# Optimization experiments

Measured on AMD Instinct MI355X. Metric: run time of the kernel, lower is better.

## Reference

```python
import jax, jax.numpy as jnp
import numpy as np

B, T, D = 16, 2048, 512  # batch, max timesteps, input_size == output_size
H = D                    # output_size


def setup_inputs() -> dict:
    key = jax.random.key(0)
    k1, k2, k3, k4 = jax.random.split(key, 4)
    x = jax.random.normal(k1, (B, T, D), dtype=jnp.float32)
    lengths = jax.random.randint(k2, (B,), 1, T + 1)
    lengths = jnp.sort(lengths)[::-1].at[0].set(T)  # descending, max == T (pack_padded contract)
    W_in = jax.random.normal(k3, (6 * H, D), dtype=jnp.float32) * (1.0 / np.sqrt(D))
    b_in = jax.random.normal(k4, (6 * H,), dtype=jnp.float32) * 0.01
    return {"x": x, "lengths": lengths, "W_in": W_in, "b_in": b_in}


def reference(x, lengths, W_in, b_in):
    # Faithful to the given source: input_linearity is applied to BOTH the
    # timestep input and the previous hidden state (requires input_size == output_size).
    Bx, Tx, Dx = x.shape
    Wt = W_in.T  # [D, 6H]

    xt_all = jnp.transpose(x, (1, 0, 2))                               # [T, B, D]
    mask_all = (jnp.arange(Tx)[:, None] < lengths[None, :])            # [T, B]

    def step(carry, inputs):
        h, c = carry                 # [B, H] each
        x_t, mask = inputs           # [B, D], [B]
        pi = x_t @ Wt + b_in         # [B, 6H]
        ps = h @ Wt + b_in           # [B, 6H]  (input_linearity on state, per source)
        g = pi[:, :5 * H] + ps[:, :5 * H]
        i_g = jax.nn.sigmoid(g[:, 0 * H:1 * H])
        f_g = jax.nn.sigmoid(g[:, 1 * H:2 * H])
        m_i = jnp.tanh(g[:, 2 * H:3 * H])
        o_g = jax.nn.sigmoid(g[:, 3 * H:4 * H])
        hw_g = jax.nn.sigmoid(g[:, 4 * H:5 * H])
        mem = i_g * m_i + f_g * c
        out = o_g * jnp.tanh(mem)
        out = hw_g * out + (1.0 - hw_g) * pi[:, 5 * H:6 * H]
        m = mask[:, None].astype(x.dtype)
        out = out * m                # padded rows produce 0, state zeroed (matches source)
        mem = mem * m
        return (out, mem), out

    h0 = jnp.zeros((Bx, H), dtype=x.dtype)
    c0 = jnp.zeros((Bx, H), dtype=x.dtype)
    _, outs = jax.lax.scan(step, (h0, c0), (xt_all, mask_all))  # outs: [T, B, H]
    return jnp.transpose(outs, (1, 0, 2))                       # [B, T, H] padded output
```

## Files before the change

kernel.cpp:

```cpp
#include <hip/hip_runtime.h>


#define NG 64
#define BLK 256
#define BB 16
#define TT 2048
#define DD 512
#define HHH 512
#define CC 8

typedef _Float16 f16;
typedef _Float16 f16x4 __attribute__((ext_vector_type(4)));
typedef _Float16 f16x8 __attribute__((ext_vector_type(8)));
typedef float f32x4 __attribute__((ext_vector_type(4)));
typedef unsigned long long u64;

__device__ __forceinline__ float sigf(float v) {
  return 1.0f / (1.0f + __expf(-v));
}
__device__ __forceinline__ float tanhfast(float v) {
  return 2.0f / (1.0f + __expf(-2.0f * v)) - 1.0f;
}

__device__ __forceinline__ f16 h_lo(u64 w) {
  return __builtin_bit_cast(f16, (unsigned short)(w & 0xffffu));
}
__device__ __forceinline__ f16 h_hi(u64 w) {
  return __builtin_bit_cast(f16, (unsigned short)((w >> 16) & 0xffffu));
}

__global__ __launch_bounds__(BLK, 1) void lstm_scan(
    const float* __restrict__ x, const int* __restrict__ lengths,
    const float* __restrict__ W, const float* __restrict__ bias,
    float* __restrict__ out,
    u64* __restrict__ hex , int repmask) {
  __shared__ f16 u_sw[BB * DD];
  __shared__ f16 h_sw[BB * DD];
  __shared__ float gbuf[4 * 16 * 17];
  __shared__ float cbuf[BB * CC];

  const int tid = threadIdx.x;
  const int wg = blockIdx.x;
  const int wave = tid >> 6;
  const int lane = tid & 63;
  const int q = lane >> 4;
  const int n16 = lane & 15;
  const int nrep = repmask + 1;

  f16x8 bW[16];
  {
    int grow = 0;
    bool valid = true;
    if (wave < 3) {
      int gate = 2 * wave + (n16 >> 3);
      grow = gate * HHH + wg * CC + (n16 & 7);
    } else if (n16 < 8) {
      grow = 5 * HHH + wg * CC + n16;
    } else {
      valid = false;
    }
    const float* wr = W + (size_t)grow * DD;
#pragma unroll
    for (int kk = 0; kk < 16; ++kk) {
      f16x8 v;
      if (valid) {
        const float* p = wr + kk * 32 + q * 8;
#pragma unroll
        for (int j = 0; j < 8; ++j) v[j] = (f16)p[j];
      } else {
#pragma unroll
        for (int j = 0; j < 8; ++j) v[j] = (f16)0.0f;
      }
      bW[kk] = v;
    }
  }

  int soffv[8], pidx[8];
  size_t xcm[8];
#pragma unroll
  for (int i = 0; i < 8; ++i) {
    int e = (tid + i * BLK) * 4;
    int m = e >> 9;
    int k = e & 511;
    pidx[i] = m * 256 + (k >> 1);
    xcm[i] = (size_t)m * TT * DD + k;
    int kk = k >> 5, qq = (k >> 3) & 3, j0 = k & 7;
    int L = qq * 16 + m;
    soffv[i] = (kk * 64 + (L ^ kk)) * 8 + j0;
  }

  const int eb = tid >> 3;
  const int en = tid & 7;
  float bb0 = 0, bb1 = 0, bb2 = 0, bb3 = 0, bb4 = 0, bb5 = 0;
  int mylen = 0;
  if (tid < 128) {
    int gc = wg * CC + en;
    bb0 = bias[0 * HHH + gc];
    bb1 = bias[1 * HHH + gc];
    bb2 = bias[2 * HHH + gc];
    bb3 = bias[3 * HHH + gc];
    bb4 = bias[4 * HHH + gc];
    bb5 = bias[5 * HHH + gc];
    mylen = lengths[eb];
    cbuf[tid] = 0.0f;
  }

  u64* const myrep = hex + (size_t)(wg & repmask) * 8192;

  f32x4 xv[8];
#pragma unroll
  for (int i = 0; i < 8; ++i) xv[i] = *(const f32x4*)(x + xcm[i]);

  __syncthreads();

  for (int t = 0; t < TT; ++t) {
    const u64* hb = myrep + (size_t)(t & 1) * 4096;
    const unsigned wtag = (unsigned)t;
    u64 w0[8], w1[8];
    for (;;) {
#pragma unroll
      for (int i = 0; i < 8; ++i) {
        w0[i] = __hip_atomic_load(hb + pidx[i], __ATOMIC_RELAXED,
                                  __HIP_MEMORY_SCOPE_AGENT);
        w1[i] = __hip_atomic_load(hb + pidx[i] + 1, __ATOMIC_RELAXED,
                                  __HIP_MEMORY_SCOPE_AGENT);
      }
      unsigned bad = 0;
#pragma unroll
      for (int i = 0; i < 8; ++i)
        bad |= ((unsigned)(w0[i] >> 32) ^ wtag) |
               ((unsigned)(w1[i] >> 32) ^ wtag);
      if (bad == 0) break;
    }

#pragma unroll
    for (int i = 0; i < 8; ++i) {
      f16x4 hv;
      hv[0] = h_lo(w0[i]);
      hv[1] = h_hi(w0[i]);
      hv[2] = h_lo(w1[i]);
      hv[3] = h_hi(w1[i]);
      f16x4 uv;
#pragma unroll
      for (int j = 0; j < 4; ++j) uv[j] = (f16)xv[i][j] + hv[j];
      *(f16x4*)(u_sw + soffv[i]) = uv;
      *(f16x4*)(h_sw + soffv[i]) = hv;
    }
    __syncthreads();

    f32x4 acc0 = {0.f, 0.f, 0.f, 0.f}, acc1 = {0.f, 0.f, 0.f, 0.f};
    f32x4 acc2 = {0.f, 0.f, 0.f, 0.f}, acc3 = {0.f, 0.f, 0.f, 0.f};
    const f16* asrc = (wave < 3) ? u_sw : h_sw;
#pragma unroll
    for (int kk = 0; kk < 16; kk += 4) {
      f16x8 a0 = *(const f16x8*)(asrc + (kk * 64 + (lane ^ kk)) * 8);
      f16x8 a1 =
          *(const f16x8*)(asrc + ((kk + 1) * 64 + (lane ^ (kk + 1))) * 8);
      f16x8 a2 =
          *(const f16x8*)(asrc + ((kk + 2) * 64 + (lane ^ (kk + 2))) * 8);
      f16x8 a3 =
          *(const f16x8*)(asrc + ((kk + 3) * 64 + (lane ^ (kk + 3))) * 8);
      acc0 = __builtin_amdgcn_mfma_f32_16x16x32_f16(a0, bW[kk], acc0, 0, 0, 0);
      acc1 =
          __builtin_amdgcn_mfma_f32_16x16x32_f16(a1, bW[kk + 1], acc1, 0, 0, 0);
      acc2 =
          __builtin_amdgcn_mfma_f32_16x16x32_f16(a2, bW[kk + 2], acc2, 0, 0, 0);
      acc3 =
          __builtin_amdgcn_mfma_f32_16x16x32_f16(a3, bW[kk + 3], acc3, 0, 0, 0);
    }
#pragma unroll
    for (int r = 0; r < 4; ++r)
      gbuf[wave * 272 + (q * 4 + r) * 17 + n16] =
          (acc0[r] + acc1[r]) + (acc2[r] + acc3[r]);
    __syncthreads();

    if (tid < 128) {
      float g0 = gbuf[0 * 272 + eb * 17 + en] + 2.f * bb0;
      float g1 = gbuf[0 * 272 + eb * 17 + en + 8] + 2.f * bb1;
      float g2 = gbuf[1 * 272 + eb * 17 + en] + 2.f * bb2;
      float g3 = gbuf[1 * 272 + eb * 17 + en + 8] + 2.f * bb3;
      float g4 = gbuf[2 * 272 + eb * 17 + en] + 2.f * bb4;
      float p5 = gbuf[2 * 272 + eb * 17 + en + 8];
      float qv = gbuf[3 * 272 + eb * 17 + en];
      float ig = sigf(g0), fg = sigf(g1), mt = tanhfast(g2);
      float og = sigf(g3), hwv = sigf(g4);
      float pi5 = p5 - qv + bb5;
      float cold = cbuf[tid];
      float mem = ig * mt + fg * cold;
      float o1 = og * tanhfast(mem);
      float ov = hwv * o1 + (1.0f - hwv) * pi5;
      float msk = (t < mylen) ? 1.0f : 0.0f;
      ov *= msk;
      mem *= msk;
      cbuf[tid] = mem;

      unsigned hbits =
          (unsigned)__builtin_bit_cast(unsigned short, (f16)ov);
      unsigned other = (unsigned)__shfl_xor((int)hbits, 1, 64);
      u64 wv;
      if ((en & 1) == 0)
        wv = (u64)(hbits & 0xffffu) | ((u64)(other & 0xffffu) << 16) |
             ((u64)(unsigned)(t + 1) << 32);
      else
        wv = (u64)(other & 0xffffu) | ((u64)(hbits & 0xffffu) << 16) |
             ((u64)(unsigned)(t + 1) << 32);
      const int rh = (nrep + 1) >> 1;
      const int rs = (en & 1) ? rh : 0;
      const int re = (en & 1) ? nrep : rh;
      u64* pdst = hex + (size_t)rs * 8192 + (size_t)((t + 1) & 1) * 4096 +
                  eb * 256 + wg * 4 + (en >> 1);
      for (int r = rs; r < re; ++r) {
        __hip_atomic_store(pdst, wv, __ATOMIC_RELAXED,
                           __HIP_MEMORY_SCOPE_AGENT);
        pdst += 8192;
      }
      out[((size_t)eb * TT + t) * HHH + wg * CC + en] = ov;
    }

    if (t + 1 < TT) {
#pragma unroll
      for (int i = 0; i < 8; ++i)
        xv[i] = *(const f32x4*)(x + xcm[i] + (size_t)(t + 1) * DD);
    }
  }
}

extern "C" void kernel_launch(void* const* d_in, const int* in_sizes, int n_in,
                              void* d_out, int out_size, void* d_ws,
                              size_t ws_size, hipStream_t stream) {
  (void)in_sizes;
  (void)n_in;
  (void)out_size;
  const float* x = (const float*)d_in[0];
  const int* lengths = (const int*)d_in[1];
  const float* W = (const float*)d_in[2];
  const float* bias = (const float*)d_in[3];
  float* out = (float*)d_out;

  u64* hex = (u64*)d_ws;
  int nrep = 1;
  if (ws_size >= (size_t)16 * 8192 * sizeof(u64))
    nrep = 16;
  else if (ws_size >= (size_t)8 * 8192 * sizeof(u64))
    nrep = 8;
  hipMemsetAsync(d_ws, 0, (size_t)nrep * 8192 * sizeof(u64), stream);

  lstm_scan<<<dim3(NG), dim3(BLK), 0, stream>>>(x, lengths, W, bias, out, hex,
                                                nrep - 1);
}
```

Before: 7.987 ms.

## Halve workgroup count, double columns per group with eight waves

Changes the persistent scan from 64 workgroups of 4 waves, each owning 8 hidden columns, to 32 workgroups of 8 waves owning 16 columns. Seven waves each compute one full 16-column gate block with MFMA, and the eighth wave sits idle. Fewer workgroups means fewer participants in the per-timestep global handshake, fewer polling readers per replica, and wider stores per group. The hidden-state replica count is also capped at 8 instead of 16. The trade-off is more work per group on the serial critical path and an idle wave.

```diff
diff --git a/kernel.cpp b/kernel.cpp
--- a/kernel.cpp
+++ b/kernel.cpp
@@ -1,13 +1,13 @@
 #include <hip/hip_runtime.h>
 
 
-#define NG 64
-#define BLK 256
+#define NG 32
+#define BLK 512
 #define BB 16
 #define TT 2048
 #define DD 512
 #define HHH 512
-#define CC 8
+#define CC 16
 
 typedef _Float16 f16;
 typedef _Float16 f16x4 __attribute__((ext_vector_type(4)));
@@ -36,7 +36,7 @@
     u64* __restrict__ hex , int repmask) {
   __shared__ f16 u_sw[BB * DD];
   __shared__ f16 h_sw[BB * DD];
-  __shared__ float gbuf[4 * 16 * 17];
+  __shared__ float gbuf[7 * 16 * 17];
   __shared__ float cbuf[BB * CC];
 
   const int tid = threadIdx.x;
@@ -48,37 +48,23 @@
   const int nrep = repmask + 1;
 
   f16x8 bW[16];
-  {
-    int grow = 0;
-    bool valid = true;
-    if (wave < 3) {
-      int gate = 2 * wave + (n16 >> 3);
-      grow = gate * HHH + wg * CC + (n16 & 7);
-    } else if (n16 < 8) {
-      grow = 5 * HHH + wg * CC + n16;
-    } else {
-      valid = false;
-    }
+  if (wave < 7) {
+    int grow = (wave < 6 ? wave : 5) * HHH + wg * CC + n16;
     const float* wr = W + (size_t)grow * DD;
 #pragma unroll
     for (int kk = 0; kk < 16; ++kk) {
       f16x8 v;
-      if (valid) {
-        const float* p = wr + kk * 32 + q * 8;
-#pragma unroll
-        for (int j = 0; j < 8; ++j) v[j] = (f16)p[j];
-      } else {
-#pragma unroll
-        for (int j = 0; j < 8; ++j) v[j] = (f16)0.0f;
-      }
+      const float* p = wr + kk * 32 + q * 8;
+#pragma unroll
+      for (int j = 0; j < 8; ++j) v[j] = (f16)p[j];
       bW[kk] = v;
     }
   }
 
-  int soffv[8], pidx[8];
-  size_t xcm[8];
-#pragma unroll
-  for (int i = 0; i < 8; ++i) {
+  int soffv[4], pidx[4];
+  size_t xcm[4];
+#pragma unroll
+  for (int i = 0; i < 4; ++i) {
     int e = (tid + i * BLK) * 4;
     int m = e >> 9;
     int k = e & 511;
@@ -89,11 +75,11 @@
     soffv[i] = (kk * 64 + (L ^ kk)) * 8 + j0;
   }
 
-  const int eb = tid >> 3;
-  const int en = tid & 7;
+  const int eb = tid >> 4;
+  const int en = tid & 15;
   float bb0 = 0, bb1 = 0, bb2 = 0, bb3 = 0, bb4 = 0, bb5 = 0;
   int mylen = 0;
-  if (tid < 128) {
+  if (tid < 256) {
     int gc = wg * CC + en;
     bb0 = bias[0 * HHH + gc];
     bb1 = bias[1 * HHH + gc];
@@ -107,19 +93,19 @@
 
   u64* const myrep = hex + (size_t)(wg & repmask) * 8192;
 
-  f32x4 xv[8];
-#pragma unroll
-  for (int i = 0; i < 8; ++i) xv[i] = *(const f32x4*)(x + xcm[i]);
+  f32x4 xv[4];
+#pragma unroll
+  for (int i = 0; i < 4; ++i) xv[i] = *(const f32x4*)(x + xcm[i]);
 
   __syncthreads();
 
   for (int t = 0; t < TT; ++t) {
     const u64* hb = myrep + (size_t)(t & 1) * 4096;
     const unsigned wtag = (unsigned)t;
-    u64 w0[8], w1[8];
+    u64 w0[4], w1[4];
     for (;;) {
 #pragma unroll
-      for (int i = 0; i < 8; ++i) {
+      for (int i = 0; i < 4; ++i) {
         w0[i] = __hip_atomic_load(hb + pidx[i], __ATOMIC_RELAXED,
                                   __HIP_MEMORY_SCOPE_AGENT);
         w1[i] = __hip_atomic_load(hb + pidx[i] + 1, __ATOMIC_RELAXED,
@@ -127,14 +113,14 @@
       }
       unsigned bad = 0;
 #pragma unroll
-      for (int i = 0; i < 8; ++i)
+      for (int i = 0; i < 4; ++i)
         bad |= ((unsigned)(w0[i] >> 32) ^ wtag) |
                ((unsigned)(w1[i] >> 32) ^ wtag);
       if (bad == 0) break;
     }
 
 #pragma unroll
-    for (int i = 0; i < 8; ++i) {
+    for (int i = 0; i < 4; ++i) {
       f16x4 hv;
       hv[0] = h_lo(w0[i]);
       hv[1] = h_hi(w0[i]);
@@ -148,40 +134,43 @@
     }
     __syncthreads();
 
-    f32x4 acc0 = {0.f, 0.f, 0.f, 0.f}, acc1 = {0.f, 0.f, 0.f, 0.f};
-    f32x4 acc2 = {0.f, 0.f, 0.f, 0.f}, acc3 = {0.f, 0.f, 0.f, 0.f};
-    const f16* asrc = (wave < 3) ? u_sw : h_sw;
-#pragma unroll
-    for (int kk = 0; kk < 16; kk += 4) {
-      f16x8 a0 = *(const f16x8*)(asrc + (kk * 64 + (lane ^ kk)) * 8);
-      f16x8 a1 =
-          *(const f16x8*)(asrc + ((kk + 1) * 64 + (lane ^ (kk + 1))) * 8);
-      f16x8 a2 =
-          *(const f16x8*)(asrc + ((kk + 2) * 64 + (lane ^ (kk + 2))) * 8);
-      f16x8 a3 =
-          *(const f16x8*)(asrc + ((kk + 3) * 64 + (lane ^ (kk + 3))) * 8);
-      acc0 = __builtin_amdgcn_mfma_f32_16x16x32_f16(a0, bW[kk], acc0, 0, 0, 0);
-      acc1 =
-          __builtin_amdgcn_mfma_f32_16x16x32_f16(a1, bW[kk + 1], acc1, 0, 0, 0);
-      acc2 =
-          __builtin_amdgcn_mfma_f32_16x16x32_f16(a2, bW[kk + 2], acc2, 0, 0, 0);
-      acc3 =
-          __builtin_amdgcn_mfma_f32_16x16x32_f16(a3, bW[kk + 3], acc3, 0, 0, 0);
-    }
-#pragma unroll
-    for (int r = 0; r < 4; ++r)
-      gbuf[wave * 272 + (q * 4 + r) * 17 + n16] =
-          (acc0[r] + acc1[r]) + (acc2[r] + acc3[r]);
+    if (wave < 7) {
+      f32x4 acc0 = {0.f, 0.f, 0.f, 0.f}, acc1 = {0.f, 0.f, 0.f, 0.f};
+      f32x4 acc2 = {0.f, 0.f, 0.f, 0.f}, acc3 = {0.f, 0.f, 0.f, 0.f};
+      const f16* asrc = (wave == 6) ? h_sw : u_sw;
+#pragma unroll
+      for (int kk = 0; kk < 16; kk += 4) {
+        f16x8 a0 = *(const f16x8*)(asrc + (kk * 64 + (lane ^ kk)) * 8);
+        f16x8 a1 =
+            *(const f16x8*)(asrc + ((kk + 1) * 64 + (lane ^ (kk + 1))) * 8);
+        f16x8 a2 =
+            *(const f16x8*)(asrc + ((kk + 2) * 64 + (lane ^ (kk + 2))) * 8);
+        f16x8 a3 =
+            *(const f16x8*)(asrc + ((kk + 3) * 64 + (lane ^ (kk + 3))) * 8);
+        acc0 =
+            __builtin_amdgcn_mfma_f32_16x16x32_f16(a0, bW[kk], acc0, 0, 0, 0);
+        acc1 = __builtin_amdgcn_mfma_f32_16x16x32_f16(a1, bW[kk + 1], acc1, 0,
+                                                      0, 0);
+        acc2 = __builtin_amdgcn_mfma_f32_16x16x32_f16(a2, bW[kk + 2], acc2, 0,
+                                                      0, 0);
+        acc3 = __builtin_amdgcn_mfma_f32_16x16x32_f16(a3, bW[kk + 3], acc3, 0,
+                                                      0, 0);
+      }
+#pragma unroll
+      for (int r = 0; r < 4; ++r)
+        gbuf[wave * 272 + (q * 4 + r) * 17 + n16] =
+            (acc0[r] + acc1[r]) + (acc2[r] + acc3[r]);
+    }
     __syncthreads();
 
-    if (tid < 128) {
+    if (tid < 256) {
       float g0 = gbuf[0 * 272 + eb * 17 + en] + 2.f * bb0;
-      float g1 = gbuf[0 * 272 + eb * 17 + en + 8] + 2.f * bb1;
-      float g2 = gbuf[1 * 272 + eb * 17 + en] + 2.f * bb2;
-      float g3 = gbuf[1 * 272 + eb * 17 + en + 8] + 2.f * bb3;
-      float g4 = gbuf[2 * 272 + eb * 17 + en] + 2.f * bb4;
-      float p5 = gbuf[2 * 272 + eb * 17 + en + 8];
-      float qv = gbuf[3 * 272 + eb * 17 + en];
+      float g1 = gbuf[1 * 272 + eb * 17 + en] + 2.f * bb1;
+      float g2 = gbuf[2 * 272 + eb * 17 + en] + 2.f * bb2;
+      float g3 = gbuf[3 * 272 + eb * 17 + en] + 2.f * bb3;
+      float g4 = gbuf[4 * 272 + eb * 17 + en] + 2.f * bb4;
+      float p5 = gbuf[5 * 272 + eb * 17 + en];
+      float qv = gbuf[6 * 272 + eb * 17 + en];
       float ig = sigf(g0), fg = sigf(g1), mt = tanhfast(g2);
       float og = sigf(g3), hwv = sigf(g4);
       float pi5 = p5 - qv + bb5;
@@ -208,7 +197,7 @@
       const int rs = (en & 1) ? rh : 0;
       const int re = (en & 1) ? nrep : rh;
       u64* pdst = hex + (size_t)rs * 8192 + (size_t)((t + 1) & 1) * 4096 +
-                  eb * 256 + wg * 4 + (en >> 1);
+                  eb * 256 + wg * (CC / 2) + (en >> 1);
       for (int r = rs; r < re; ++r) {
         __hip_atomic_store(pdst, wv, __ATOMIC_RELAXED,
                            __HIP_MEMORY_SCOPE_AGENT);
@@ -219,7 +208,7 @@
 
     if (t + 1 < TT) {
 #pragma unroll
-      for (int i = 0; i < 8; ++i)
+      for (int i = 0; i < 4; ++i)
         xv[i] = *(const f32x4*)(x + xcm[i] + (size_t)(t + 1) * DD);
     }
   }
@@ -238,11 +227,7 @@
   float* out = (float*)d_out;
 
   u64* hex = (u64*)d_ws;
-  int nrep = 1;
-  if (ws_size >= (size_t)16 * 8192 * sizeof(u64))
-    nrep = 16;
-  else if (ws_size >= (size_t)8 * 8192 * sizeof(u64))
-    nrep = 8;
+  int nrep = (ws_size >= (size_t)8 * 8192 * sizeof(u64)) ? 8 : 1;
   hipMemsetAsync(d_ws, 0, (size_t)nrep * 8192 * sizeof(u64), stream);
 
   lstm_scan<<<dim3(NG), dim3(BLK), 0, stream>>>(x, lengths, W, bias, out, hex,
```

After: 6.463 ms. 19.1% less time.
